# Performance work log

Measured on AMD Instinct MI355X. Metric: run time of the kernel, lower is better.

## Reference

```python
import jax, jax.numpy as jnp
import numpy as np

N_NODES, N_EDGES, B = 100000, 200000, 2048
ND, ED, HID, OUT, HEADS = 64, 16, 512, 512, 4

# dummy-graph topology: central node 0 -> features 1..6, plus self loops (GATv2 default)
D_SRC = jnp.array([0, 0, 0, 0, 0, 0, 0, 1, 2, 3, 4, 5, 6])
D_DST = jnp.array([1, 2, 3, 4, 5, 6, 0, 1, 2, 3, 4, 5, 6])


def setup_inputs() -> dict:
    key = jax.random.key(0)
    ks = jax.random.split(key, 40)
    p = lambda k, sh: (jax.random.normal(k, sh, dtype=jnp.float32) * 0.05)
    inp = {
        'x': jax.random.normal(ks[0], (N_NODES, ND), dtype=jnp.float32),
        'edge_index': jax.random.randint(ks[1], (2, N_EDGES), 0, N_NODES),
        'edge_attr': jax.random.normal(ks[2], (N_EDGES, ED), dtype=jnp.float32),
        'batch': jnp.sort(jax.random.randint(ks[3], (N_NODES,), 0, B)),
        'ecfp': jax.random.uniform(ks[4], (B, OUT), dtype=jnp.float32),
        'topo': jax.random.uniform(ks[5], (B, OUT), dtype=jnp.float32),
        'maccs': jax.random.uniform(ks[6], (B, OUT), dtype=jnp.float32),
        'estate': jax.random.uniform(ks[7], (B, OUT), dtype=jnp.float32),
        'rdkit2d': jax.random.normal(ks[8], (B, OUT), dtype=jnp.float32),
        'phar2d': jax.random.normal(ks[9], (B, OUT), dtype=jnp.float32),
        # GINEConv 1: nn = Linear(ND, HID); edge proj Linear(ED, ND)
        'g1_W': p(ks[10], (ND, HID)), 'g1_b': p(ks[11], (HID,)),
        'e1_W': p(ks[12], (ED, ND)), 'e1_b': p(ks[13], (ND,)),
        'bn1_g': jnp.ones((HID,), jnp.float32), 'bn1_b': jnp.zeros((HID,), jnp.float32),
        # GINEConv 2: nn = Linear(HID, OUT); edge proj Linear(ED, HID)
        'g2_W': p(ks[14], (HID, OUT)), 'g2_b': p(ks[15], (OUT,)),
        'e2_W': p(ks[16], (ED, HID)), 'e2_b': p(ks[17], (HID,)),
        'bn2_g': jnp.ones((OUT,), jnp.float32), 'bn2_b': jnp.zeros((OUT,), jnp.float32),
        # GATv2Conv 1: OUT -> HID, heads, concat=False
        'gat1_Wl': p(ks[18], (OUT, HEADS * HID)), 'gat1_bl': p(ks[19], (HEADS * HID,)),
        'gat1_Wr': p(ks[20], (OUT, HEADS * HID)), 'gat1_br': p(ks[21], (HEADS * HID,)),
        'gat1_att': p(ks[22], (HEADS, HID)), 'gat1_bias': p(ks[23], (HID,)),
        'bn3_g': jnp.ones((HID,), jnp.float32), 'bn3_b': jnp.zeros((HID,), jnp.float32),
        # GATv2Conv 2: HID -> HID
        'gat2_Wl': p(ks[24], (HID, HEADS * HID)), 'gat2_bl': p(ks[25], (HEADS * HID,)),
        'gat2_Wr': p(ks[26], (HID, HEADS * HID)), 'gat2_br': p(ks[27], (HEADS * HID,)),
        'gat2_att': p(ks[28], (HEADS, HID)), 'gat2_bias': p(ks[29], (HID,)),
        'bn4_g': jnp.ones((HID,), jnp.float32), 'bn4_b': jnp.zeros((HID,), jnp.float32),
        'fc_W': p(ks[30], (HID, 1)), 'fc_b': p(ks[31], (1,)),
    }
    return inp


def _bn_eval(h, g, b):
    # PyG BatchNorm in eval mode with fresh running stats (mean=0, var=1)
    return g * (h * (1.0 / np.sqrt(1.0 + 1e-5))) + b


def _gatv2(z, Wl, bl, Wr, br, att, bias):
    # z: [B, 7, Cin]; GATv2Conv with self-loops, concat=False (mean over heads)
    Bn, Nn, _ = z.shape
    Hh, Co = att.shape
    gl = (z @ Wl + bl).reshape(Bn, Nn, Hh, Co)  # source transform
    gr = (z @ Wr + br).reshape(Bn, Nn, Hh, Co)  # target transform
    e = jax.nn.leaky_relu(gl[:, D_SRC] + gr[:, D_DST], 0.2)  # [B, 13, H, Co]
    logits = jnp.einsum('behc,hc->beh', e, att)  # [B, 13, H]

    def seg_softmax(lg):
        m = jax.ops.segment_max(lg, D_DST, num_segments=7)
        ex = jnp.exp(lg - m[D_DST])
        s = jax.ops.segment_sum(ex, D_DST, num_segments=7)
        return ex / s[D_DST]

    alpha = jax.vmap(seg_softmax)(logits)  # [B, 13, H]
    msg = gl[:, D_SRC] * alpha[..., None]  # [B, 13, H, Co]
    out = jax.vmap(lambda mm: jax.ops.segment_sum(mm, D_DST, num_segments=7))(msg)
    return out.mean(axis=2) + bias  # [B, 7, Co]


def reference(x, edge_index, edge_attr, batch, ecfp, topo, maccs, estate, rdkit2d, phar2d,
              g1_W, g1_b, e1_W, e1_b, bn1_g, bn1_b,
              g2_W, g2_b, e2_W, e2_b, bn2_g, bn2_b,
              gat1_Wl, gat1_bl, gat1_Wr, gat1_br, gat1_att, gat1_bias, bn3_g, bn3_b,
              gat2_Wl, gat2_bl, gat2_Wr, gat2_br, gat2_att, gat2_bias, bn4_g, bn4_b,
              fc_W, fc_b):
    N = x.shape[0]
    Bg = ecfp.shape[0]
    src, dst = edge_index[0], edge_index[1]
    # GINEConv 1: msg = relu(x_j + W_e e), sum-aggr, out = Lin(x + aggr) (eps=0)
    m = jax.nn.relu(x[src] + (edge_attr @ e1_W + e1_b))
    h = (x + jax.ops.segment_sum(m, dst, num_segments=N)) @ g1_W + g1_b
    h = jax.nn.relu(_bn_eval(h, bn1_g, bn1_b))  # dropout = identity (eval)
    # GINEConv 2
    m2 = jax.nn.relu(h[src] + (edge_attr @ e2_W + e2_b))
    h2 = (h + jax.ops.segment_sum(m2, dst, num_segments=N)) @ g2_W + g2_b
    h2 = jax.nn.relu(_bn_eval(h2, bn2_g, bn2_b))
    # global mean pool
    sums = jax.ops.segment_sum(h2, batch, num_segments=Bg)
    cnts = jax.ops.segment_sum(jnp.ones((N,), h2.dtype), batch, num_segments=Bg)
    graph_out = sums / jnp.maximum(cnts, 1.0)[:, None]  # [B, OUT]
    # batched 7-node dummy graphs (node 0 = graph embedding, 1..6 = features)
    xn = jnp.stack([graph_out, ecfp, topo, maccs, estate, rdkit2d, phar2d], axis=1)
    z = _gatv2(xn, gat1_Wl, gat1_bl, gat1_Wr, gat1_br, gat1_att, gat1_bias)
    z = jax.nn.relu(_bn_eval(z, bn3_g, bn3_b))
    z = _gatv2(z, gat2_Wl, gat2_bl, gat2_Wr, gat2_br, gat2_att, gat2_bias)
    z = jax.nn.relu(_bn_eval(z, bn4_g, bn4_b))
    return z[:, 0, :] @ fc_W + fc_b  # [B, 1]
```

## Files before the change

kernel.cpp:

```cpp
#include <hip/hip_runtime.h>
#include <hip/hip_bf16.h>

#define N_NODESC 100000
#define N_EDGESC 200000
#define BG 2048
#define NDIM 64
#define EDIM 16

typedef __bf16 bf16x8 __attribute__((ext_vector_type(8)));
typedef float f32x4 __attribute__((ext_vector_type(4)));

static __device__ __forceinline__ float bn_inv() { return 0.9999950000374997f; }

__device__ __forceinline__ void gl2lds16(const void* g, void* l) {
    __builtin_amdgcn_global_load_lds(
        (const __attribute__((address_space(1))) unsigned int*)g,
        (__attribute__((address_space(3))) unsigned int*)l, 16, 0, 0);
}

__global__ void zero_f4(float4* __restrict__ p, int n4) {
    int i = blockIdx.x * 256 + threadIdx.x;
    if (i < n4) p[i] = make_float4(0.f, 0.f, 0.f, 0.f);
}
__global__ void zero_int(int* __restrict__ p, int n) {
    int i = blockIdx.x * 256 + threadIdx.x;
    if (i < n) p[i] = 0;
}
__global__ void zero_out(float* __restrict__ p, int n) {
    int i = blockIdx.x * 256 + threadIdx.x;
    if (i < n) p[i] = 0.f;
}

__global__ void hist_dst(const int* __restrict__ dst, int* __restrict__ deg) {
    int i = blockIdx.x * 256 + threadIdx.x;
    if (i < N_EDGESC) atomicAdd(&deg[dst[i]], 1);
}
__global__ void scan_bsums(const int* __restrict__ deg, int* __restrict__ bsum, int n) {
    __shared__ int ls[256];
    int b = blockIdx.x, t = threadIdx.x;
    int s = 0;
#pragma unroll
    for (int j = 0; j < 4; j++) {
        int i = b * 1024 + t * 4 + j;
        if (i < n) s += deg[i];
    }
    ls[t] = s;
    __syncthreads();
    for (int off = 128; off; off >>= 1) {
        if (t < off) ls[t] += ls[t + off];
        __syncthreads();
    }
    if (t == 0) bsum[b] = ls[0];
}
__global__ void scan_top(int* __restrict__ bsum, int nb, int* __restrict__ total) {
    if (threadIdx.x == 0) {
        int acc = 0;
        for (int i = 0; i < nb; i++) { int v = bsum[i]; bsum[i] = acc; acc += v; }
        *total = acc;
    }
}
__global__ void scan_final(const int* __restrict__ deg, const int* __restrict__ bsum,
                           int* __restrict__ rowptr, int* __restrict__ cursor, int n) {
    __shared__ int ls[256];
    int b = blockIdx.x, t = threadIdx.x;
    int v[4], s = 0;
#pragma unroll
    for (int j = 0; j < 4; j++) {
        int i = b * 1024 + t * 4 + j;
        v[j] = (i < n) ? deg[i] : 0;
        s += v[j];
    }
    ls[t] = s;
    __syncthreads();
    int run = s;
    for (int off = 1; off < 256; off <<= 1) {
        int add = (t >= off) ? ls[t - off] : 0;
        __syncthreads();
        ls[t] += add;
        __syncthreads();
    }
    int excl = ls[t] - run + bsum[b];
#pragma unroll
    for (int j = 0; j < 4; j++) {
        int i = b * 1024 + t * 4 + j;
        if (i < n) { rowptr[i] = excl; cursor[i] = excl; excl += v[j]; }
    }
}
__global__ void scatter_eid(const int* __restrict__ dst, int* __restrict__ cursor,
                            int* __restrict__ eid) {
    int e = blockIdx.x * 256 + threadIdx.x;
    if (e < N_EDGESC) {
        int p = atomicAdd(&cursor[dst[e]], 1);
        eid[p] = e;
    }
}

__global__ void transpose_w(const float* __restrict__ W, __hip_bfloat16* __restrict__ hi,
                            int K, int N) {
    __shared__ float t[64][65];
    int k0 = blockIdx.x * 64, n0 = blockIdx.y * 64;
    int tid = threadIdx.x, tx = tid & 63, ty = tid >> 6;
    for (int r = ty; r < 64; r += 4) t[r][tx] = W[(size_t)(k0 + r) * N + n0 + tx];
    __syncthreads();
    for (int r = ty; r < 64; r += 4)
        hi[(size_t)(n0 + r) * K + k0 + tx] = __float2bfloat16(t[tx][r]);
}

__global__ void concat_bias(const float* __restrict__ a, const float* __restrict__ b,
                            float* __restrict__ o) {
    int i = blockIdx.x * 256 + threadIdx.x;
    if (i < 2048) { o[i] = a[i]; o[2048 + i] = b[i]; }
}

#define G1_NPW 8
__global__ __launch_bounds__(256, 2) void gine1_gather(
    const float* __restrict__ x, const int* __restrict__ srcv, const float* __restrict__ ea,
    const float* __restrict__ e1W, const float* __restrict__ e1b,
    const int* __restrict__ rowptr, const int* __restrict__ eid,
    __hip_bfloat16* __restrict__ xin) {
    int tid = threadIdx.x;
    int wave = tid >> 6, lane = tid & 63;
    float wreg[16];
#pragma unroll
    for (int k = 0; k < 16; k++) wreg[k] = e1W[k * 64 + lane];
    float bb = e1b[lane];
    int nbase = (blockIdx.x * 4 + wave) * G1_NPW;
#pragma unroll 1
    for (int it = 0; it < G1_NPW; it++) {
        int n = nbase + it;
        if (n >= N_NODESC) return;
        float acc = x[(size_t)n * 64 + lane];
        int beg = rowptr[n], end = rowptr[n + 1];
        for (int idx = beg; idx < end; idx++) {
            int e = eid[idx], s = srcv[e];
            const float4* ef = (const float4*)(ea + (size_t)e * 16);
            float4 e0 = ef[0], e1 = ef[1], e2 = ef[2], e3 = ef[3];
            float p = bb;
            p = fmaf(e0.x, wreg[0], p);  p = fmaf(e0.y, wreg[1], p);
            p = fmaf(e0.z, wreg[2], p);  p = fmaf(e0.w, wreg[3], p);
            p = fmaf(e1.x, wreg[4], p);  p = fmaf(e1.y, wreg[5], p);
            p = fmaf(e1.z, wreg[6], p);  p = fmaf(e1.w, wreg[7], p);
            p = fmaf(e2.x, wreg[8], p);  p = fmaf(e2.y, wreg[9], p);
            p = fmaf(e2.z, wreg[10], p); p = fmaf(e2.w, wreg[11], p);
            p = fmaf(e3.x, wreg[12], p); p = fmaf(e3.y, wreg[13], p);
            p = fmaf(e3.z, wreg[14], p); p = fmaf(e3.w, wreg[15], p);
            acc += fmaxf(x[(size_t)s * 64 + lane] + p, 0.f);
        }
        xin[(size_t)n * 64 + lane] = __float2bfloat16(acc);
    }
}

#define G2_NPB 16
__global__ __launch_bounds__(256, 2) void gine2_gather(
    const __hip_bfloat16* __restrict__ h, const int* __restrict__ srcv,
    const float* __restrict__ ea, const float* __restrict__ e2W,
    const float* __restrict__ e2b, const int* __restrict__ rowptr,
    const int* __restrict__ eid, __hip_bfloat16* __restrict__ a2, int n0, int n1) {
    int tid = threadIdx.x;
    int half = tid >> 7, lt = tid & 127;
    float wreg[4][16], breg[4];
#pragma unroll
    for (int j = 0; j < 4; j++) {
        int c = lt * 4 + j;
        breg[j] = e2b[c];
#pragma unroll
        for (int k = 0; k < 16; k++) wreg[j][k] = e2W[k * 512 + c];
    }
    int nbase = n0 + blockIdx.x * G2_NPB + half;
#pragma unroll 1
    for (int it = 0; it < G2_NPB / 2; it++) {
        int n = nbase + it * 2;
        if (n >= n1) return;
        short4 hv = *(const short4*)((const short*)(h + (size_t)n * 512) + lt * 4);
        const __hip_bfloat16* hb = (const __hip_bfloat16*)&hv;
        float acc[4];
#pragma unroll
        for (int j = 0; j < 4; j++) acc[j] = __bfloat162float(hb[j]);
        int beg = rowptr[n], end = rowptr[n + 1];
        for (int idx = beg; idx < end; idx++) {
            int e = eid[idx], s = srcv[e];
            const float4* ef = (const float4*)(ea + (size_t)e * 16);
            float4 e0 = ef[0], e1 = ef[1], e2v = ef[2], e3 = ef[3];
            short4 sv = *(const short4*)((const short*)(h + (size_t)s * 512) + lt * 4);
            const __hip_bfloat16* sb = (const __hip_bfloat16*)&sv;
#pragma unroll
            for (int j = 0; j < 4; j++) {
                float p = breg[j];
                p = fmaf(e0.x, wreg[j][0], p);  p = fmaf(e0.y, wreg[j][1], p);
                p = fmaf(e0.z, wreg[j][2], p);  p = fmaf(e0.w, wreg[j][3], p);
                p = fmaf(e1.x, wreg[j][4], p);  p = fmaf(e1.y, wreg[j][5], p);
                p = fmaf(e1.z, wreg[j][6], p);  p = fmaf(e1.w, wreg[j][7], p);
                p = fmaf(e2v.x, wreg[j][8], p); p = fmaf(e2v.y, wreg[j][9], p);
                p = fmaf(e2v.z, wreg[j][10], p);p = fmaf(e2v.w, wreg[j][11], p);
                p = fmaf(e3.x, wreg[j][12], p); p = fmaf(e3.y, wreg[j][13], p);
                p = fmaf(e3.z, wreg[j][14], p); p = fmaf(e3.w, wreg[j][15], p);
                acc[j] += fmaxf(__bfloat162float(sb[j]) + p, 0.f);
            }
        }
        __hip_bfloat16 o[4];
#pragma unroll
        for (int j = 0; j < 4; j++) o[j] = __float2bfloat16(acc[j]);
        *(short4*)((short*)(a2 + (size_t)(n - n0) * 512) + lt * 4) = *(const short4*)o;
    }
}

template <int MODE>
__global__ __launch_bounds__(256, 4) void mfma_gemm(
    const __hip_bfloat16* __restrict__ A, const __hip_bfloat16* __restrict__ Bhi,
    int M, int K, int N, const float* __restrict__ bias, const float* __restrict__ bng,
    const float* __restrict__ bnb, const int* __restrict__ batch,
    float* __restrict__ psum, __hip_bfloat16* __restrict__ Cout) {
    __shared__ short As[128 * 32];
    __shared__ short Bh[128 * 32];
    int r0 = blockIdx.y * 128;
    int n0 = blockIdx.x * 128;
    int tid = threadIdx.x;
    int lane = tid & 63;
    int wv = tid >> 6;
    int wm = (wv >> 1) * 64, wn = (wv & 1) * 64;

    f32x4 acc[4][4];
#pragma unroll
    for (int i = 0; i < 4; i++)
#pragma unroll
        for (int j = 0; j < 4; j++) acc[i][j] = (f32x4){0.f, 0.f, 0.f, 0.f};

    int rowA0 = tid >> 2, cbA0 = tid & 3;
    int rowA1 = (tid + 256) >> 2, cbA1 = tid & 3;
    for (int k0 = 0; k0 < K; k0 += 32) {
        __syncthreads();
        {
            int g0 = r0 + rowA0; if (g0 >= M) g0 = M - 1;
            int g1 = r0 + rowA1; if (g1 >= M) g1 = M - 1;
            gl2lds16(A + (size_t)g0 * K + k0 + cbA0 * 8, As + wv * 512);
            gl2lds16(A + (size_t)g1 * K + k0 + cbA1 * 8, As + 2048 + wv * 512);
            gl2lds16(Bhi + (size_t)(n0 + rowA0) * K + k0 + cbA0 * 8, Bh + wv * 512);
            gl2lds16(Bhi + (size_t)(n0 + rowA1) * K + k0 + cbA1 * 8, Bh + 2048 + wv * 512);
        }
        __syncthreads();
        int fi = lane & 15, kb = (lane >> 4) * 8;
        bf16x8 af[4], bhf[4];
#pragma unroll
        for (int mi = 0; mi < 4; mi++)
            af[mi] = *(const bf16x8*)(As + (wm + mi * 16 + fi) * 32 + kb);
#pragma unroll
        for (int ni = 0; ni < 4; ni++)
            bhf[ni] = *(const bf16x8*)(Bh + (wn + ni * 16 + fi) * 32 + kb);
#pragma unroll
        for (int mi = 0; mi < 4; mi++)
#pragma unroll
            for (int ni = 0; ni < 4; ni++)
                acc[mi][ni] = __builtin_amdgcn_mfma_f32_16x16x32_bf16(af[mi], bhf[ni],
                                                                     acc[mi][ni], 0, 0, 0);
    }
    int col_l = lane & 15, quad = lane >> 4;
#pragma unroll
    for (int mi = 0; mi < 4; mi++) {
        int rbase = r0 + wm + mi * 16 + quad * 4;
#pragma unroll
        for (int ni = 0; ni < 4; ni++) {
            int gcol = n0 + wn + ni * 16 + col_l;
            if (MODE == 0) {
                float b0 = bias[gcol];
#pragma unroll
                for (int reg = 0; reg < 4; reg++) {
                    int grow = rbase + reg;
                    if (grow < M)
                        Cout[(size_t)grow * N + gcol] = __float2bfloat16(acc[mi][ni][reg] + b0);
                }
            } else {
                float b0 = bias[gcol], g0 = bng[gcol], bb0 = bnb[gcol];
                float vv[4];
#pragma unroll
                for (int reg = 0; reg < 4; reg++)
                    vv[reg] = fmaxf(fmaf((acc[mi][ni][reg] + b0) * bn_inv(), g0, bb0), 0.f);
                if (MODE == 1) {
#pragma unroll
                    for (int reg = 0; reg < 4; reg++) {
                        int grow = rbase + reg;
                        if (grow < M) Cout[(size_t)grow * 512 + gcol] = __float2bfloat16(vv[reg]);
                    }
                } else {
                    if (rbase + 3 < M && batch[rbase] == batch[rbase + 3]) {
                        atomicAdd(&psum[(size_t)batch[rbase] * 512 + gcol],
                                  (vv[0] + vv[1]) + (vv[2] + vv[3]));
                    } else {
#pragma unroll
                        for (int reg = 0; reg < 4; reg++) {
                            int grow = rbase + reg;
                            if (grow < M)
                                atomicAdd(&psum[(size_t)batch[grow] * 512 + gcol], vv[reg]);
                        }
                    }
                }
            }
        }
    }
}

__global__ void count_nodes(const int* __restrict__ batch, float* __restrict__ cnt) {
    int i = blockIdx.x * 256 + threadIdx.x;
    if (i < N_NODESC) atomicAdd(&cnt[batch[i]], 1.0f);
}

__global__ void build_xn(const float* __restrict__ psum, const float* __restrict__ cnt,
                         const float* __restrict__ ecfp, const float* __restrict__ topo,
                         const float* __restrict__ maccs, const float* __restrict__ estate,
                         const float* __restrict__ rdkit2d, const float* __restrict__ phar2d,
                         __hip_bfloat16* __restrict__ xn) {
    int i = blockIdx.x * 256 + threadIdx.x;
    if (i >= BG * 512) return;
    int bidx = i >> 9, c = i & 511;
    float cv = fmaxf(cnt[bidx], 1.0f);
    __hip_bfloat16* o = xn + (size_t)bidx * 7 * 512;
    o[c] = __float2bfloat16(psum[i] / cv);
    o[512 + c] = __float2bfloat16(ecfp[i]);
    o[2 * 512 + c] = __float2bfloat16(topo[i]);
    o[3 * 512 + c] = __float2bfloat16(maccs[i]);
    o[4 * 512 + c] = __float2bfloat16(estate[i]);
    o[5 * 512 + c] = __float2bfloat16(rdkit2d[i]);
    o[6 * 512 + c] = __float2bfloat16(phar2d[i]);
}

__global__ void gat_attn(const __hip_bfloat16* __restrict__ cg,
                         const float* __restrict__ att, const float* __restrict__ bias,
                         const float* __restrict__ bng, const float* __restrict__ bnb,
                         __hip_bfloat16* __restrict__ zout) {
    int b = blockIdx.x;
    int tid = threadIdx.x;
    int wave = tid >> 6, lane = tid & 63;
    __shared__ float logits[13][4];
    __shared__ float alpha[13][4];
    const size_t base = (size_t)b * 7 * 4096;
    for (int p = wave; p < 52; p += 4) {
        int e = p >> 2, hh = p & 3;
        int se = (e < 7) ? 0 : (e - 6);
        int de = (e < 6) ? (e + 1) : ((e == 6) ? 0 : (e - 6));
        const __hip_bfloat16* glp = cg + base + (size_t)se * 4096 + hh * 512;
        const __hip_bfloat16* grp = cg + base + (size_t)de * 4096 + 2048 + hh * 512;
        const float* ap = att + hh * 512;
        float s = 0.f;
#pragma unroll
        for (int j = 0; j < 8; j++) {
            int c = lane + j * 64;
            float v = __bfloat162float(glp[c]) + __bfloat162float(grp[c]);
            v = (v >= 0.f) ? v : 0.2f * v;
            s = fmaf(v, ap[c], s);
        }
#pragma unroll
        for (int off = 32; off; off >>= 1) s += __shfl_down(s, off);
        if (lane == 0) logits[e][hh] = s;
    }
    __syncthreads();
    if (tid < 24) {
        int n = 1 + (tid >> 2), hh = tid & 3;
        float la = logits[n - 1][hh], lb = logits[6 + n][hh];
        float m = fmaxf(la, lb);
        float ea = __expf(la - m), eb = __expf(lb - m);
        float inv = 1.f / (ea + eb);
        alpha[n - 1][hh] = ea * inv;
        alpha[6 + n][hh] = eb * inv;
    } else if (tid < 28) {
        alpha[6][tid & 3] = 1.f;
    }
    __syncthreads();
    for (int i = tid; i < 7 * 512; i += 256) {
        int n = i >> 9, c = i & 511;
        float v = 0.f;
        if (n == 0) {
#pragma unroll
            for (int hh = 0; hh < 4; hh++)
                v = fmaf(alpha[6][hh],
                         __bfloat162float(cg[base + (size_t)hh * 512 + c]), v);
        } else {
#pragma unroll
            for (int hh = 0; hh < 4; hh++) {
                v = fmaf(alpha[n - 1][hh],
                         __bfloat162float(cg[base + (size_t)hh * 512 + c]), v);
                v = fmaf(alpha[6 + n][hh],
                         __bfloat162float(cg[base + (size_t)n * 4096 + hh * 512 + c]), v);
            }
        }
        v = fmaf(v, 0.25f, bias[c]);
        v = fmaf(v * bn_inv(), bng[c], bnb[c]);
        zout[(size_t)b * 7 * 512 + i] = __float2bfloat16(fmaxf(v, 0.f));
    }
}

__global__ void final_fc(const __hip_bfloat16* __restrict__ z, const float* __restrict__ fcW,
                         const float* __restrict__ fcb, float* __restrict__ out) {
    int b = blockIdx.x * 4 + (threadIdx.x >> 6);
    int lane = threadIdx.x & 63;
    if (b >= BG) return;
    const __hip_bfloat16* row = z + (size_t)b * 7 * 512;
    float s = 0.f;
#pragma unroll
    for (int j = 0; j < 8; j++)
        s = fmaf(__bfloat162float(row[lane + j * 64]), fcW[lane + j * 64], s);
#pragma unroll
    for (int off = 32; off; off >>= 1) s += __shfl_down(s, off);
    if (lane == 0) out[b] = s + fcb[0];
}

extern "C" void kernel_launch(void* const* d_in, const int* in_sizes, int n_in,
                              void* d_out, int out_size, void* d_ws, size_t ws_size,
                              hipStream_t stream) {
    const float* x = (const float*)d_in[0];
    const int* eidx = (const int*)d_in[1];
    const float* eattr = (const float*)d_in[2];
    const int* batch = (const int*)d_in[3];
    const float* ecfp = (const float*)d_in[4];
    const float* topo = (const float*)d_in[5];
    const float* maccs = (const float*)d_in[6];
    const float* estate = (const float*)d_in[7];
    const float* rdkit2d = (const float*)d_in[8];
    const float* phar2d = (const float*)d_in[9];
    const float* g1_W = (const float*)d_in[10];
    const float* g1_b = (const float*)d_in[11];
    const float* e1_W = (const float*)d_in[12];
    const float* e1_b = (const float*)d_in[13];
    const float* bn1_g = (const float*)d_in[14];
    const float* bn1_b = (const float*)d_in[15];
    const float* g2_W = (const float*)d_in[16];
    const float* g2_b = (const float*)d_in[17];
    const float* e2_W = (const float*)d_in[18];
    const float* e2_b = (const float*)d_in[19];
    const float* bn2_g = (const float*)d_in[20];
    const float* bn2_b = (const float*)d_in[21];
    const float* gat1_Wl = (const float*)d_in[22];
    const float* gat1_bl = (const float*)d_in[23];
    const float* gat1_Wr = (const float*)d_in[24];
    const float* gat1_br = (const float*)d_in[25];
    const float* gat1_att = (const float*)d_in[26];
    const float* gat1_bias = (const float*)d_in[27];
    const float* bn3_g = (const float*)d_in[28];
    const float* bn3_b = (const float*)d_in[29];
    const float* gat2_Wl = (const float*)d_in[30];
    const float* gat2_bl = (const float*)d_in[31];
    const float* gat2_Wr = (const float*)d_in[32];
    const float* gat2_br = (const float*)d_in[33];
    const float* gat2_att = (const float*)d_in[34];
    const float* gat2_bias = (const float*)d_in[35];
    const float* bn4_g = (const float*)d_in[36];
    const float* bn4_b = (const float*)d_in[37];
    const float* fc_W = (const float*)d_in[38];
    const float* fc_b = (const float*)d_in[39];
    float* out = (float*)d_out;

    const size_t NEEDED = 194682880ull;
    if (ws_size < NEEDED) {
        zero_out<<<(BG + 255) / 256, 256, 0, stream>>>(out, BG);
        return;
    }
    char* w = (char*)d_ws;
    __hip_bfloat16* H = (__hip_bfloat16*)w;
    __hip_bfloat16* CG = (__hip_bfloat16*)w;
    __hip_bfloat16* A2 = (__hip_bfloat16*)(w + 102400000);
    __hip_bfloat16* GW12 = (__hip_bfloat16*)(w + 117440512);
    __hip_bfloat16* GW34 = (__hip_bfloat16*)(w + 121634816);
    __hip_bfloat16* Z1B = (__hip_bfloat16*)(w + 125829120);
    float* B12 = (float*)(w + 140509184);
    float* B34 = (float*)(w + 140525568);

    char* C = w + 161120256;
    __hip_bfloat16* XIN = (__hip_bfloat16*)C;
    __hip_bfloat16* XNB = (__hip_bfloat16*)C;
    __hip_bfloat16* Z2B = (__hip_bfloat16*)(C + 14680064);
    int* ROWPTR = (int*)(C + 14680064);
    int* CURSOR = (int*)(C + 15080192);
    int* EID = (int*)(C + 15480320);
    int* DEG = (int*)(C + 16280320);
    __hip_bfloat16* G1W = (__hip_bfloat16*)(C + 16680320);
    __hip_bfloat16* G2W = (__hip_bfloat16*)(C + 16745856);
    int* BSUM = (int*)(C + 17270144);

    float* PS = (float*)(w + 190480384);
    float* PC = (float*)(w + 194674688);

    const int* src = eidx;
    const int* dst = eidx + N_EDGESC;

    zero_int<<<(N_NODESC + 255) / 256, 256, 0, stream>>>(DEG, N_NODESC);
    zero_f4<<<(BG * 512 / 4 + 255) / 256, 256, 0, stream>>>((float4*)PS, BG * 512 / 4);
    zero_f4<<<(BG / 4 + 255) / 256, 256, 0, stream>>>((float4*)PC, BG / 4);
    hist_dst<<<(N_EDGESC + 255) / 256, 256, 0, stream>>>(dst, DEG);
    const int NB = (N_NODESC + 1023) / 1024;
    scan_bsums<<<NB, 256, 0, stream>>>(DEG, BSUM, N_NODESC);
    scan_top<<<1, 64, 0, stream>>>(BSUM, NB, ROWPTR + N_NODESC);
    scan_final<<<NB, 256, 0, stream>>>(DEG, BSUM, ROWPTR, CURSOR, N_NODESC);
    scatter_eid<<<(N_EDGESC + 255) / 256, 256, 0, stream>>>(dst, CURSOR, EID);

    transpose_w<<<dim3(1, 8), 256, 0, stream>>>(g1_W, G1W, 64, 512);
    transpose_w<<<dim3(8, 8), 256, 0, stream>>>(g2_W, G2W, 512, 512);

    gine1_gather<<<(N_NODESC + 4 * G1_NPW - 1) / (4 * G1_NPW), 256, 0, stream>>>(
        x, src, eattr, e1_W, e1_b, ROWPTR, EID, XIN);
    mfma_gemm<1><<<dim3(4, (N_NODESC + 127) / 128), 256, 0, stream>>>(
        XIN, G1W, N_NODESC, 64, 512, g1_b, bn1_g, bn1_b, nullptr, nullptr, H);
    count_nodes<<<(N_NODESC + 255) / 256, 256, 0, stream>>>(batch, PC);

    for (int c0n = 0; c0n < N_NODESC; c0n += 50000) {
        int c1n = c0n + 50000;
        int rows = 50000;
        gine2_gather<<<(rows + G2_NPB - 1) / G2_NPB, 256, 0, stream>>>(
            H, src, eattr, e2_W, e2_b, ROWPTR, EID, A2, c0n, c1n);
        mfma_gemm<2><<<dim3(4, (rows + 127) / 128), 256, 0, stream>>>(
            A2, G2W, rows, 512, 512, g2_b, bn2_g, bn2_b, batch + c0n, PS, nullptr);
    }

    transpose_w<<<dim3(8, 32), 256, 0, stream>>>(gat1_Wl, GW12, 512, 2048);
    transpose_w<<<dim3(8, 32), 256, 0, stream>>>(gat1_Wr, GW12 + (size_t)2048 * 512, 512, 2048);
    transpose_w<<<dim3(8, 32), 256, 0, stream>>>(gat2_Wl, GW34, 512, 2048);
    transpose_w<<<dim3(8, 32), 256, 0, stream>>>(gat2_Wr, GW34 + (size_t)2048 * 512, 512, 2048);
    concat_bias<<<8, 256, 0, stream>>>(gat1_bl, gat1_br, B12);
    concat_bias<<<8, 256, 0, stream>>>(gat2_bl, gat2_br, B34);

    build_xn<<<(BG * 512) / 256, 256, 0, stream>>>(PS, PC, ecfp, topo, maccs, estate,
                                                   rdkit2d, phar2d, XNB);
    const int MGAT = BG * 7;
    dim3 ggrid(4096 / 128, MGAT / 128);
    mfma_gemm<0><<<ggrid, 256, 0, stream>>>(XNB, GW12, MGAT, 512, 4096, B12,
                                            nullptr, nullptr, nullptr, nullptr, CG);
    gat_attn<<<BG, 256, 0, stream>>>(CG, gat1_att, gat1_bias, bn3_g, bn3_b, Z1B);
    mfma_gemm<0><<<ggrid, 256, 0, stream>>>(Z1B, GW34, MGAT, 512, 4096, B34,
                                            nullptr, nullptr, nullptr, nullptr, CG);
    gat_attn<<<BG, 256, 0, stream>>>(CG, gat2_att, gat2_bias, bn4_g, bn4_b, Z2B);
    final_fc<<<BG / 4, 256, 0, stream>>>(Z2B, fc_W, fc_b, out);
}
```

Measured before the change: 1.034 ms.

## Double GEMM K-tile to 64 and remap blocks into grouped row tiles

The MFMA GEMM now stages 64-wide K slices into LDS per iteration, halving the number of barrier pairs and issuing more loads per sync, with two 32-wide MFMA sub-steps per slice. Launches switch to a 1D grid that a block maps to (row tile, column tile) in groups of 8 row tiles per column sweep. This keeps A row tiles and B column tiles hot in L2. LDS use doubles and the occupancy hint drops from 4 to 3 blocks per CU. Padded blocks past the last row tile exit early.

New measurement: 1.059 ms. 2.4% more time.

```diff
diff --git a/kernel.cpp b/kernel.cpp
--- a/kernel.cpp
+++ b/kernel.cpp
@@ -205,15 +205,23 @@
 }
 
 template <int MODE>
-__global__ __launch_bounds__(256, 4) void mfma_gemm(
+__global__ __launch_bounds__(256, 3) void mfma_gemm(
     const __hip_bfloat16* __restrict__ A, const __hip_bfloat16* __restrict__ Bhi,
     int M, int K, int N, const float* __restrict__ bias, const float* __restrict__ bng,
     const float* __restrict__ bnb, const int* __restrict__ batch,
     float* __restrict__ psum, __hip_bfloat16* __restrict__ Cout) {
-    __shared__ short As[128 * 32];
-    __shared__ short Bh[128 * 32];
-    int r0 = blockIdx.y * 128;
-    int n0 = blockIdx.x * 128;
+    __shared__ short As[128 * 64];
+    __shared__ short Bh[128 * 64];
+    int nRT = (M + 127) >> 7;
+    int nCT = N >> 7;
+    int per = nCT << 3;
+    int id = blockIdx.x;
+    int grp = id / per, wi = id % per;
+    int ct = wi >> 3, rx = wi & 7;
+    int rt = grp * 8 + rx;
+    if (rt >= nRT) return;
+    int r0 = rt * 128, n0 = ct * 128;
+
     int tid = threadIdx.x;
     int lane = tid & 63;
     int wv = tid >> 6;
@@ -225,33 +233,34 @@
 #pragma unroll
         for (int j = 0; j < 4; j++) acc[i][j] = (f32x4){0.f, 0.f, 0.f, 0.f};
 
-    int rowA0 = tid >> 2, cbA0 = tid & 3;
-    int rowA1 = (tid + 256) >> 2, cbA1 = tid & 3;
-    for (int k0 = 0; k0 < K; k0 += 32) {
+    int fi = lane & 15, kb = (lane >> 4) * 8;
+    for (int k0 = 0; k0 < K; k0 += 64) {
         __syncthreads();
-        {
-            int g0 = r0 + rowA0; if (g0 >= M) g0 = M - 1;
-            int g1 = r0 + rowA1; if (g1 >= M) g1 = M - 1;
-            gl2lds16(A + (size_t)g0 * K + k0 + cbA0 * 8, As + wv * 512);
-            gl2lds16(A + (size_t)g1 * K + k0 + cbA1 * 8, As + 2048 + wv * 512);
-            gl2lds16(Bhi + (size_t)(n0 + rowA0) * K + k0 + cbA0 * 8, Bh + wv * 512);
-            gl2lds16(Bhi + (size_t)(n0 + rowA1) * K + k0 + cbA1 * 8, Bh + 2048 + wv * 512);
+#pragma unroll
+        for (int j = 0; j < 4; j++) {
+            int i = tid + j * 256;
+            int row = i >> 3, cb = i & 7;
+            int gA = r0 + row; if (gA >= M) gA = M - 1;
+            gl2lds16(A + (size_t)gA * K + k0 + cb * 8, As + wv * 512 + j * 2048);
+            gl2lds16(Bhi + (size_t)(n0 + row) * K + k0 + cb * 8, Bh + wv * 512 + j * 2048);
         }
         __syncthreads();
-        int fi = lane & 15, kb = (lane >> 4) * 8;
-        bf16x8 af[4], bhf[4];
-#pragma unroll
-        for (int mi = 0; mi < 4; mi++)
-            af[mi] = *(const bf16x8*)(As + (wm + mi * 16 + fi) * 32 + kb);
-#pragma unroll
-        for (int ni = 0; ni < 4; ni++)
-            bhf[ni] = *(const bf16x8*)(Bh + (wn + ni * 16 + fi) * 32 + kb);
-#pragma unroll
-        for (int mi = 0; mi < 4; mi++)
+#pragma unroll
+        for (int kh = 0; kh < 64; kh += 32) {
+            bf16x8 af[4], bhf[4];
+#pragma unroll
+            for (int mi = 0; mi < 4; mi++)
+                af[mi] = *(const bf16x8*)(As + (wm + mi * 16 + fi) * 64 + kb + kh);
 #pragma unroll
             for (int ni = 0; ni < 4; ni++)
-                acc[mi][ni] = __builtin_amdgcn_mfma_f32_16x16x32_bf16(af[mi], bhf[ni],
-                                                                     acc[mi][ni], 0, 0, 0);
+                bhf[ni] = *(const bf16x8*)(Bh + (wn + ni * 16 + fi) * 64 + kb + kh);
+#pragma unroll
+            for (int mi = 0; mi < 4; mi++)
+#pragma unroll
+                for (int ni = 0; ni < 4; ni++)
+                    acc[mi][ni] = __builtin_amdgcn_mfma_f32_16x16x32_bf16(
+                        af[mi], bhf[ni], acc[mi][ni], 0, 0, 0);
+        }
     }
     int col_l = lane & 15, quad = lane >> 4;
 #pragma unroll
@@ -296,6 +305,12 @@
             }
         }
     }
+}
+
+static inline int gemm_grid(int M, int N) {
+    int nRT = (M + 127) >> 7, nCT = N >> 7;
+    int nGrp = (nRT + 7) >> 3;
+    return nGrp * 8 * nCT;
 }
 
 __global__ void count_nodes(const int* __restrict__ batch, float* __restrict__ cnt) {
@@ -495,7 +510,7 @@
 
     gine1_gather<<<(N_NODESC + 4 * G1_NPW - 1) / (4 * G1_NPW), 256, 0, stream>>>(
         x, src, eattr, e1_W, e1_b, ROWPTR, EID, XIN);
-    mfma_gemm<1><<<dim3(4, (N_NODESC + 127) / 128), 256, 0, stream>>>(
+    mfma_gemm<1><<<gemm_grid(N_NODESC, 512), 256, 0, stream>>>(
         XIN, G1W, N_NODESC, 64, 512, g1_b, bn1_g, bn1_b, nullptr, nullptr, H);
     count_nodes<<<(N_NODESC + 255) / 256, 256, 0, stream>>>(batch, PC);
 
@@ -504,7 +519,7 @@
         int rows = 50000;
         gine2_gather<<<(rows + G2_NPB - 1) / G2_NPB, 256, 0, stream>>>(
             H, src, eattr, e2_W, e2_b, ROWPTR, EID, A2, c0n, c1n);
-        mfma_gemm<2><<<dim3(4, (rows + 127) / 128), 256, 0, stream>>>(
+        mfma_gemm<2><<<gemm_grid(rows, 512), 256, 0, stream>>>(
             A2, G2W, rows, 512, 512, g2_b, bn2_g, bn2_b, batch + c0n, PS, nullptr);
     }
 
@@ -518,12 +533,11 @@
     build_xn<<<(BG * 512) / 256, 256, 0, stream>>>(PS, PC, ecfp, topo, maccs, estate,
                                                    rdkit2d, phar2d, XNB);
     const int MGAT = BG * 7;
-    dim3 ggrid(4096 / 128, MGAT / 128);
-    mfma_gemm<0><<<ggrid, 256, 0, stream>>>(XNB, GW12, MGAT, 512, 4096, B12,
-                                            nullptr, nullptr, nullptr, nullptr, CG);
+    mfma_gemm<0><<<gemm_grid(MGAT, 4096), 256, 0, stream>>>(
+        XNB, GW12, MGAT, 512, 4096, B12, nullptr, nullptr, nullptr, nullptr, CG);
     gat_attn<<<BG, 256, 0, stream>>>(CG, gat1_att, gat1_bias, bn3_g, bn3_b, Z1B);
-    mfma_gemm<0><<<ggrid, 256, 0, stream>>>(Z1B, GW34, MGAT, 512, 4096, B34,
-                                            nullptr, nullptr, nullptr, nullptr, CG);
+    mfma_gemm<0><<<gemm_grid(MGAT, 4096), 256, 0, stream>>>(
+        Z1B, GW34, MGAT, 512, 4096, B34, nullptr, nullptr, nullptr, nullptr, CG);
     gat_attn<<<BG, 256, 0, stream>>>(CG, gat2_att, gat2_bias, bn4_g, bn4_b, Z2B);
     final_fc<<<BG / 4, 256, 0, stream>>>(Z2B, fc_W, fc_b, out);
 }
```
